# Kernel optimization log

Hardware: AMD Instinct MI355X
Metric: run time of the kernel (lower is better)

## Reference

```python
import jax, jax.numpy as jnp
import numpy as np

BLOCKSIZE = 64
# Fixed NF4 codebook (bitsandbytes normal-float 4-bit quantiles)
NF4_CODE = jnp.array([
    -1.0, -0.6961928009986877, -0.5250730514526367, -0.39491748809814453,
    -0.28444138169288635, -0.18477343022823334, -0.09105003625154495, 0.0,
    0.07958029955625534, 0.16093020141124725, 0.24611230194568634,
    0.33791524171829224, 0.44070982933044434, 0.5626170039176941,
    0.7229568362236023, 1.0], dtype=jnp.float32)


def setup_inputs() -> dict:
    key = jax.random.key(0)
    k1, k2, k3, k4 = jax.random.split(key, 4)
    B, IN, OUT = 32, 4096, 14336
    x = jax.random.normal(k1, (B, IN), dtype=jnp.float32)
    codes = jax.random.randint(k2, (OUT, IN), 0, 16, dtype=jnp.int32)
    absmax = jax.random.uniform(k3, (OUT * IN // BLOCKSIZE,), dtype=jnp.float32)
    bias = jax.random.normal(k4, (OUT,), dtype=jnp.float32)
    return {"x": x, "codes": codes, "absmax": absmax, "bias": bias}


def reference(x, codes, absmax, bias):
    out_f, in_f = codes.shape
    # Dequantize: codebook lookup then per-block (64) absmax scaling
    w = NF4_CODE[codes].reshape(-1, BLOCKSIZE) * absmax[:, None]  # [nblocks, 64]
    w = w.reshape(out_f, in_f)
    # y = x @ W^T + bias  (matmul_4bit semantics)
    return jnp.einsum('bi,oi->bo', x, w) + bias
```

## Files before the change

### kernel.cpp

```cpp
#include <hip/hip_runtime.h>
#include <stddef.h>
#include <stdint.h>

#define B_   32
#define IN_  4096
#define OUT_ 14336

typedef short v8s __attribute__((ext_vector_type(8)));
typedef float v4f __attribute__((ext_vector_type(4)));

__device__ __constant__ float c_nf4[16] = {
    -1.0f, -0.6961928009986877f, -0.5250730514526367f, -0.39491748809814453f,
    -0.28444138169288635f, -0.18477343022823334f, -0.09105003625154495f, 0.0f,
    0.07958029955625534f, 0.16093020141124725f, 0.24611230194568634f,
    0.33791524171829224f, 0.44070982933044434f, 0.5626170039176941f,
    0.7229568362236023f, 1.0f};

__device__ __forceinline__ unsigned f2bf_u(float f) {
    union { float f; unsigned u; } v; v.f = f;
    return (v.u + 0x7FFFu + ((v.u >> 16) & 1u)) >> 16;
}
__device__ __forceinline__ unsigned pack2(float lo, float hi) {
    return f2bf_u(lo) | (f2bf_u(hi) << 16);
}

__global__ __launch_bounds__(256) void prep(const float* __restrict__ x,
                                            unsigned* __restrict__ xB) {
    int t  = blockIdx.x * 256 + threadIdx.x;
    int kt = t >> 7;
    int bt = (t >> 6) & 1;
    int l  = t & 63;
    int b  = bt * 16 + (l & 15);
    int k0 = kt * 32 + (l >> 4) * 8;
    const float* xr = x + (size_t)b * IN_ + k0;
    float4 a = *(const float4*)xr;
    float4 c = *(const float4*)(xr + 4);
    uint4 w;
    w.x = pack2(a.x, a.y);
    w.y = pack2(a.z, a.w);
    w.z = pack2(c.x, c.y);
    w.w = pack2(c.z, c.w);
    *(uint4*)(xB + (size_t)t * 4) = w;
}

__global__ __launch_bounds__(256) void nf4_mfma(
    const int* __restrict__ codes, const float* __restrict__ absmax,
    const unsigned* __restrict__ xB, const float* __restrict__ bias,
    float* __restrict__ out) {
    __shared__ float lut[16];
    if (threadIdx.x < 16) lut[threadIdx.x] = c_nf4[threadIdx.x];
    __syncthreads();

    const int w  = threadIdx.x >> 6;
    const int l  = threadIdx.x & 63;
    const int o0 = blockIdx.x * 64 + w * 16;
    const int m  = l & 15;
    const int q  = l >> 4;

    const int*   crow  = codes + (size_t)(o0 + m) * IN_ + q * 8;
    const float* amrow = absmax + (size_t)(o0 + m) * 64;
    const uint4* xbp   = (const uint4*)xB + l;

    v4f acc0 = {0.f, 0.f, 0.f, 0.f};
    v4f acc1 = {0.f, 0.f, 0.f, 0.f};

#pragma unroll 4
    for (int kt = 0; kt < 128; ++kt) {
        int4 c0 = *(const int4*)(crow + (size_t)kt * 32);
        int4 c1 = *(const int4*)(crow + (size_t)kt * 32 + 4);
        uint4 b0 = xbp[(size_t)kt * 128];
        uint4 b1 = xbp[(size_t)kt * 128 + 64];
        float am = amrow[kt >> 1];

        union { uint4 u; v8s v; } a, f0, f1;
        a.u.x = pack2(lut[c0.x] * am, lut[c0.y] * am);
        a.u.y = pack2(lut[c0.z] * am, lut[c0.w] * am);
        a.u.z = pack2(lut[c1.x] * am, lut[c1.y] * am);
        a.u.w = pack2(lut[c1.z] * am, lut[c1.w] * am);
        f0.u = b0;
        f1.u = b1;
        acc0 = __builtin_amdgcn_mfma_f32_16x16x32_bf16(a.v, f0.v, acc0, 0, 0, 0);
        acc1 = __builtin_amdgcn_mfma_f32_16x16x32_bf16(a.v, f1.v, acc1, 0, 0, 0);
    }

    const int bc = l & 15;
    const int ob = o0 + q * 4;
#pragma unroll
    for (int r = 0; r < 4; ++r) {
        float bv = bias[ob + r];
        out[(size_t)bc * OUT_ + ob + r]        = acc0[r] + bv;
        out[(size_t)(bc + 16) * OUT_ + ob + r] = acc1[r] + bv;
    }
}

extern "C" void kernel_launch(void* const* d_in, const int* in_sizes, int n_in,
                              void* d_out, int out_size, void* d_ws, size_t ws_size,
                              hipStream_t stream) {
    const float* x      = (const float*)d_in[0];
    const int*   codes  = (const int*)d_in[1];
    const float* absmax = (const float*)d_in[2];
    const float* bias   = (const float*)d_in[3];
    float* out = (float*)d_out;
    unsigned* xB = (unsigned*)d_ws;

    prep<<<dim3(64), 256, 0, stream>>>(x, xB);
    nf4_mfma<<<dim3(OUT_ / 64), 256, 0, stream>>>(codes, absmax, xB, bias, out);
}
```

Measured before the change: 324.8 us.

## Split-K with atomics, pair-packed bf16 LUT, and post-MMA absmax scaling

The K dimension is split across 4 blocks in grid y, and partial sums are combined with atomicAdd into an output pre-filled with bias by a new init kernel. This quadruples the grid, giving more waves to hide latency on the memory-bound codes stream. Dequantization now uses a 256-entry shared LUT of packed bf16 pairs, so the per-element multiply and convert are gone. The absmax scale is applied per 64-block to the MFMA result rather than to the weights. The cost is float atomics, an extra kernel launch, and a changed rounding order.

```diff
diff --git a/kernel.cpp b/kernel.cpp
--- a/kernel.cpp
+++ b/kernel.cpp
@@ -43,53 +43,82 @@
     *(uint4*)(xB + (size_t)t * 4) = w;
 }
 
+__global__ __launch_bounds__(256) void init_out(const float* __restrict__ bias,
+                                                float* __restrict__ out) {
+    int t   = blockIdx.x * 256 + threadIdx.x;
+    int o   = (t * 4) % OUT_;
+    int row = (t * 4) / OUT_;
+    float4 bv = *(const float4*)(bias + o);
+    *(float4*)(out + (size_t)row * OUT_ + o) = bv;
+}
+
 __global__ __launch_bounds__(256) void nf4_mfma(
     const int* __restrict__ codes, const float* __restrict__ absmax,
-    const unsigned* __restrict__ xB, const float* __restrict__ bias,
-    float* __restrict__ out) {
-    __shared__ float lut[16];
-    if (threadIdx.x < 16) lut[threadIdx.x] = c_nf4[threadIdx.x];
+    const unsigned* __restrict__ xB, float* __restrict__ out) {
+    __shared__ unsigned plut[256];
+    plut[threadIdx.x] = pack2(c_nf4[threadIdx.x & 15], c_nf4[threadIdx.x >> 4]);
     __syncthreads();
 
     const int w  = threadIdx.x >> 6;
     const int l  = threadIdx.x & 63;
     const int o0 = blockIdx.x * 64 + w * 16;
+    const int kq = blockIdx.y;
     const int m  = l & 15;
     const int q  = l >> 4;
 
-    const int*   crow  = codes + (size_t)(o0 + m) * IN_ + q * 8;
-    const float* amrow = absmax + (size_t)(o0 + m) * 64;
-    const uint4* xbp   = (const uint4*)xB + l;
+    const int kt0 = kq * 32;
+    const int*   crow = codes + (size_t)(o0 + m) * IN_ + q * 8 + (size_t)kt0 * 32;
+    const uint4* xbp  = (const uint4*)xB + l + (size_t)kt0 * 128;
+    const float* amp  = absmax + (size_t)(o0 + q * 4) * 64 + kq * 16;
 
-    v4f acc0 = {0.f, 0.f, 0.f, 0.f};
-    v4f acc1 = {0.f, 0.f, 0.f, 0.f};
+    v4f main0 = {0.f, 0.f, 0.f, 0.f};
+    v4f main1 = {0.f, 0.f, 0.f, 0.f};
+    const v4f zro = {0.f, 0.f, 0.f, 0.f};
 
-#pragma unroll 4
-    for (int kt = 0; kt < 128; ++kt) {
-        int4 c0 = *(const int4*)(crow + (size_t)kt * 32);
-        int4 c1 = *(const int4*)(crow + (size_t)kt * 32 + 4);
-        uint4 b0 = xbp[(size_t)kt * 128];
-        uint4 b1 = xbp[(size_t)kt * 128 + 64];
-        float am = amrow[kt >> 1];
+#pragma unroll 2
+    for (int kb = 0; kb < 16; ++kb) {
+        const int* cA = crow + (size_t)kb * 64;
+        int4 c0 = *(const int4*)(cA);
+        int4 c1 = *(const int4*)(cA + 4);
+        int4 c2 = *(const int4*)(cA + 32);
+        int4 c3 = *(const int4*)(cA + 36);
+        uint4 b0 = xbp[(size_t)kb * 256];
+        uint4 b1 = xbp[(size_t)kb * 256 + 64];
+        uint4 b2 = xbp[(size_t)kb * 256 + 128];
+        uint4 b3 = xbp[(size_t)kb * 256 + 192];
+        float am0 = amp[kb];
+        float am1 = amp[kb + 64];
+        float am2 = amp[kb + 128];
+        float am3 = amp[kb + 192];
 
-        union { uint4 u; v8s v; } a, f0, f1;
-        a.u.x = pack2(lut[c0.x] * am, lut[c0.y] * am);
-        a.u.y = pack2(lut[c0.z] * am, lut[c0.w] * am);
-        a.u.z = pack2(lut[c1.x] * am, lut[c1.y] * am);
-        a.u.w = pack2(lut[c1.z] * am, lut[c1.w] * am);
-        f0.u = b0;
-        f1.u = b1;
-        acc0 = __builtin_amdgcn_mfma_f32_16x16x32_bf16(a.v, f0.v, acc0, 0, 0, 0);
-        acc1 = __builtin_amdgcn_mfma_f32_16x16x32_bf16(a.v, f1.v, acc1, 0, 0, 0);
+        union { uint4 u; v8s v; } aA, aB, f0, f1, f2, f3;
+        aA.u.x = plut[c0.x | (c0.y << 4)];
+        aA.u.y = plut[c0.z | (c0.w << 4)];
+        aA.u.z = plut[c1.x | (c1.y << 4)];
+        aA.u.w = plut[c1.z | (c1.w << 4)];
+        aB.u.x = plut[c2.x | (c2.y << 4)];
+        aB.u.y = plut[c2.z | (c2.w << 4)];
+        aB.u.z = plut[c3.x | (c3.y << 4)];
+        aB.u.w = plut[c3.z | (c3.w << 4)];
+        f0.u = b0; f1.u = b1; f2.u = b2; f3.u = b3;
+
+        v4f blk0 = __builtin_amdgcn_mfma_f32_16x16x32_bf16(aA.v, f0.v, zro, 0, 0, 0);
+        v4f blk1 = __builtin_amdgcn_mfma_f32_16x16x32_bf16(aA.v, f1.v, zro, 0, 0, 0);
+        blk0 = __builtin_amdgcn_mfma_f32_16x16x32_bf16(aB.v, f2.v, blk0, 0, 0, 0);
+        blk1 = __builtin_amdgcn_mfma_f32_16x16x32_bf16(aB.v, f3.v, blk1, 0, 0, 0);
+
+        main0[0] += am0 * blk0[0];  main1[0] += am0 * blk1[0];
+        main0[1] += am1 * blk0[1];  main1[1] += am1 * blk1[1];
+        main0[2] += am2 * blk0[2];  main1[2] += am2 * blk1[2];
+        main0[3] += am3 * blk0[3];  main1[3] += am3 * blk1[3];
     }
 
     const int bc = l & 15;
     const int ob = o0 + q * 4;
 #pragma unroll
     for (int r = 0; r < 4; ++r) {
-        float bv = bias[ob + r];
-        out[(size_t)bc * OUT_ + ob + r]        = acc0[r] + bv;
-        out[(size_t)(bc + 16) * OUT_ + ob + r] = acc1[r] + bv;
+        atomicAdd(&out[(size_t)bc * OUT_ + ob + r],        main0[r]);
+        atomicAdd(&out[(size_t)(bc + 16) * OUT_ + ob + r], main1[r]);
     }
 }
 
@@ -103,6 +132,7 @@
     float* out = (float*)d_out;
     unsigned* xB = (unsigned*)d_ws;
 
+    init_out<<<dim3(448), 256, 0, stream>>>(bias, out);
     prep<<<dim3(64), 256, 0, stream>>>(x, xB);
-    nf4_mfma<<<dim3(OUT_ / 64), 256, 0, stream>>>(codes, absmax, xB, bias, out);
+    nf4_mfma<<<dim3(OUT_ / 64, 4), 256, 0, stream>>>(codes, absmax, xB, out);
 }
```

Measured after the change: 335.6 us. 1.03x slower.
